# Performance work log

Measured on AMD Instinct MI355X. Metric: run time of the kernel, lower is better.

The kernel has to match this reference:

```python
import jax, jax.numpy as jnp
import numpy as np

H = 1024        # hidden_size
NH = 16         # num_heads
HD = H // NH    # head_dim
NS = 3          # num_strata


def setup_inputs() -> dict:
    key = jax.random.key(0)
    ks = jax.random.split(key, 12)
    s = 1.0 / np.sqrt(H)
    inp = {
        "hidden_states": jax.random.normal(ks[0], (2, 2048, H), dtype=jnp.float32),
        "Wq": jax.random.uniform(ks[1], (H, H), minval=-s, maxval=s, dtype=jnp.float32),
        "bq": jax.random.uniform(ks[2], (H,), minval=-s, maxval=s, dtype=jnp.float32),
        "Wk": jax.random.uniform(ks[3], (H, H), minval=-s, maxval=s, dtype=jnp.float32),
        "bk": jax.random.uniform(ks[4], (H,), minval=-s, maxval=s, dtype=jnp.float32),
        "Wv": jax.random.uniform(ks[5], (H, H), minval=-s, maxval=s, dtype=jnp.float32),
        "bv": jax.random.uniform(ks[6], (H,), minval=-s, maxval=s, dtype=jnp.float32),
        "Ws": jax.random.uniform(ks[7], (NS, H, H), minval=-s, maxval=s, dtype=jnp.float32),
        "bs": jax.random.uniform(ks[8], (NS, H), minval=-s, maxval=s, dtype=jnp.float32),
        "Wo": jax.random.uniform(ks[9], (H, H), minval=-s, maxval=s, dtype=jnp.float32),
        "bo": jax.random.uniform(ks[10], (H,), minval=-s, maxval=s, dtype=jnp.float32),
    }
    return inp


def reference(hidden_states, Wq, bq, Wk, bk, Wv, bv, Ws, bs, Wo, bo):
    B, S, _ = hidden_states.shape
    # torch nn.Linear: y = x @ W.T + b
    q = hidden_states @ Wq.T + bq
    k = hidden_states @ Wk.T + bk
    v = hidden_states @ Wv.T + bv
    # [B, NH, S, HD]
    q = q.reshape(B, S, NH, HD).transpose(0, 2, 1, 3)
    k = k.reshape(B, S, NH, HD).transpose(0, 2, 1, 3)
    v = v.reshape(B, S, NH, HD).transpose(0, 2, 1, 3)
    scores = jnp.einsum('bhqd,bhkd->bhqk', q, k) / jnp.sqrt(jnp.float32(HD))
    attn = jax.nn.softmax(scores, axis=-1)
    out = jnp.einsum('bhqk,bhkd->bhqd', attn, v)
    attn_output = out.transpose(0, 2, 1, 3).reshape(B, S, H)
    # stratum projections, averaged: [NS, B, S, H] -> mean over strata
    strata = jnp.einsum('bsh,ngh->nbsg', attn_output, Ws) + bs[:, None, None, :]
    enhanced = strata.mean(axis=0)
    output = enhanced @ Wo.T + bo
    return output
```

## Files before the change

### kernel.cpp

```cpp
#include <hip/hip_runtime.h>
#include <stdint.h>

typedef __attribute__((ext_vector_type(8))) short short8;
typedef __attribute__((ext_vector_type(4))) short short4v;
typedef __attribute__((ext_vector_type(4))) float f32x4;
typedef unsigned int u32;
typedef const __attribute__((address_space(1))) u32* gas_ptr;
typedef __attribute__((address_space(3))) u32* las_ptr;

__device__ inline short f2bf(float x) {
    u32 u = __float_as_uint(x);
    u = u + 0x7FFFu + ((u >> 16) & 1u);
    return (short)(u >> 16);
}
__device__ inline void gload16(const void* g, void* l) {
    __builtin_amdgcn_global_load_lds((gas_ptr)g, (las_ptr)l, 16, 0, 0);
}

__global__ __launch_bounds__(256) void prep(const float* __restrict__ X,
                                            const float* __restrict__ Wq,
                                            const float* __restrict__ Wk,
                                            const float* __restrict__ Wv,
                                            const float* __restrict__ Wo,
                                            const float* __restrict__ Ws,
                                            const float* __restrict__ bs,
                                            const float* __restrict__ bo,
                                            short* __restrict__ Xb,
                                            short* __restrict__ Wcat,
                                            short* __restrict__ Wob,
                                            short* __restrict__ WmT,
                                            float* __restrict__ bc) {
    __shared__ short T[64][65];
    const int tid = threadIdx.x;
    const int bid = blockIdx.x;
    if (bid < 8192) {
        const float* src;
        short* dst;
        int rel;
        if (bid < 4096)      { src = X;  dst = Xb;                rel = bid; }
        else if (bid < 5120) { src = Wq; dst = Wcat;              rel = bid - 4096; }
        else if (bid < 6144) { src = Wk; dst = Wcat + (1 << 20);  rel = bid - 5120; }
        else if (bid < 7168) { src = Wv; dst = Wcat + (2 << 20);  rel = bid - 6144; }
        else                 { src = Wo; dst = Wob;               rel = bid - 7168; }
        int i = (rel * 256 + tid) * 4;
        float4 v = *(const float4*)&src[i];
        short4v o;
        o[0] = f2bf(v.x); o[1] = f2bf(v.y); o[2] = f2bf(v.z); o[3] = f2bf(v.w);
        *(short4v*)&dst[i] = o;
    } else if (bid < 8448) {
        const int id = bid - 8192;
        const int gx = (id & 15) * 64, jy = (id >> 4) * 64;
        const int HH = 1 << 20;
        for (int e = tid; e < 4096; e += 256) {
            int j = e >> 6, g = e & 63;
            int idx = (jy + j) * 1024 + gx + g;
            float v = (Ws[idx] + Ws[idx + HH] + Ws[idx + 2 * HH]) * (1.0f / 3.0f);
            T[g][j] = f2bf(v);
        }
        __syncthreads();
        for (int e = tid; e < 4096; e += 256) {
            int g = e >> 6, j = e & 63;
            WmT[(long)(gx + g) * 1024 + jy + j] = T[g][j];
        }
    } else {
        const int lane = tid & 63;
        const int n = (bid - 8448) * 4 + (tid >> 6);
        float acc = 0.0f;
        for (int j0 = 0; j0 < 1024; j0 += 64) {
            int j = j0 + lane;
            float bm = (bs[j] + bs[j + 1024] + bs[j + 2048]) * (1.0f / 3.0f);
            acc += Wo[(long)n * 1024 + j] * bm;
        }
#pragma unroll
        for (int off = 1; off < 64; off <<= 1) acc += __shfl_xor(acc, off, 64);
        if (lane == 0) bc[n] = acc + bo[n];
    }
}

__global__ __launch_bounds__(256) void gemm_qkvwc(const short* __restrict__ Xb,
                                                  const short* __restrict__ Wcat,
                                                  const short* __restrict__ Wob,
                                                  const short* __restrict__ WmT,
                                                  const float* __restrict__ bq,
                                                  const float* __restrict__ bk,
                                                  const float* __restrict__ bv,
                                                  short* __restrict__ Qb,
                                                  short* __restrict__ Kb,
                                                  short* __restrict__ Vt,
                                                  short* __restrict__ Wc) {
    __shared__ short As[128 * 32];
    __shared__ short Bs[128 * 32];
    const int K = 1024;
    const int tid  = threadIdx.x;
    const int lane = tid & 63;
    const int wave = tid >> 6;
    const int quad = lane >> 4;
    const int l16  = lane & 15;
    const int bid = blockIdx.x;
    const short *A, *W;
    int m0, n0, sel;
    if (bid < 768) {
        m0 = (bid & 31) * 128;
        int t = bid >> 5;
        sel = t >> 3;
        n0 = (t & 7) * 128;
        A = Xb;
        W = Wcat + (long)sel * (1 << 20);
    } else {
        int w = bid - 768;
        sel = 3;
        m0 = (w >> 3) * 128;
        n0 = (w & 7) * 128;
        A = Wob;
        W = WmT;
    }
    const int wm = (wave >> 1) * 64;
    const int wn = (wave & 1) * 64;

    f32x4 acc[4][4] = {};
    const int r0 = tid >> 2, kk0 = (tid & 3) * 8;
    const int r1 = r0 + 64;

    for (int k0 = 0; k0 < K; k0 += 32) {
        gload16(&A[(long)(m0 + r0) * K + k0 + kk0], &As[wave * 512]);
        gload16(&A[(long)(m0 + r1) * K + k0 + kk0], &As[2048 + wave * 512]);
        gload16(&W[(long)(n0 + r0) * K + k0 + kk0], &Bs[wave * 512]);
        gload16(&W[(long)(n0 + r1) * K + k0 + kk0], &Bs[2048 + wave * 512]);
        __syncthreads();
        short8 af[4], bfr[4];
#pragma unroll
        for (int mi = 0; mi < 4; mi++)
            af[mi] = *(short8*)&As[(wm + mi * 16 + l16) * 32 + quad * 8];
#pragma unroll
        for (int ni = 0; ni < 4; ni++)
            bfr[ni] = *(short8*)&Bs[(wn + ni * 16 + l16) * 32 + quad * 8];
#pragma unroll
        for (int mi = 0; mi < 4; mi++)
#pragma unroll
            for (int ni = 0; ni < 4; ni++)
                acc[mi][ni] = __builtin_amdgcn_mfma_f32_16x16x32_bf16(af[mi], bfr[ni],
                                                                      acc[mi][ni], 0, 0, 0);
        __syncthreads();
    }

#pragma unroll
    for (int mi = 0; mi < 4; mi++) {
#pragma unroll
        for (int ni = 0; ni < 4; ni++) {
            const int n = n0 + wn + ni * 16 + l16;
            const int mbase = m0 + wm + mi * 16 + quad * 4;
            float bv2 = 0.0f;
            if (sel == 0) bv2 = bq[n];
            else if (sel == 1) bv2 = bk[n];
            else if (sel == 2) bv2 = bv[n];
            if (sel == 2) {
                short4v pk;
#pragma unroll
                for (int r = 0; r < 4; r++) pk[r] = f2bf(acc[mi][ni][r] + bv2);
                long addr = ((long)(mbase >> 11) << 21) + (long)n * 2048 + (mbase & 2047);
                *(short4v*)&Vt[addr] = pk;
            } else {
                short* C = (sel == 0) ? Qb : ((sel == 1) ? Kb : Wc);
#pragma unroll
                for (int r = 0; r < 4; r++)
                    C[(long)(mbase + r) * 1024 + n] = f2bf(acc[mi][ni][r] + bv2);
            }
        }
    }
}

__global__ __launch_bounds__(256) void attn_kernel(const short* __restrict__ Q,
                                                   const short* __restrict__ Kb,
                                                   const short* __restrict__ Vt,
                                                   short* __restrict__ O) {
    __shared__ short Ks[64 * 72];
    __shared__ short Vs[64 * 72];
    __shared__ short Ps[4 * 16 * 72];
    const int tid  = threadIdx.x;
    const int lane = tid & 63;
    const int wave = tid >> 6;
    const int quad = lane >> 4;
    const int l16  = lane & 15;
    const int q0 = blockIdx.x * 64;
    const int h  = blockIdx.y;
    const int b  = blockIdx.z;

    short8 qf[2];
    {
        long base = (long)(b * 2048 + q0 + wave * 16 + l16) * 1024 + h * 64 + quad * 8;
        qf[0] = *(const short8*)&Q[base];
        qf[1] = *(const short8*)&Q[base + 32];
    }

    const int sr0 = tid >> 3, sg0 = (tid & 7) * 8;
    const int sr1 = sr0 + 32;
    const short* Kp = Kb + (long)(b * 2048) * 1024 + h * 64;
    const short* Vp = Vt + ((long)b << 21) + (long)h * 64 * 2048;

    short8 pk0 = *(const short8*)&Kp[(long)sr0 * 1024 + sg0];
    short8 pk1 = *(const short8*)&Kp[(long)sr1 * 1024 + sg0];
    short8 pv0 = *(const short8*)&Vp[(long)sr0 * 2048 + sg0];
    short8 pv1 = *(const short8*)&Vp[(long)sr1 * 2048 + sg0];

    f32x4 o[4] = {};
    f32x4 ls = {};
    short8 ones;
#pragma unroll
    for (int j = 0; j < 8; j++) ones[j] = (short)0x3F80;

    for (int kt = 0; kt < 32; kt++) {
        *(short8*)&Ks[sr0 * 72 + sg0] = pk0;
        *(short8*)&Ks[sr1 * 72 + sg0] = pk1;
        *(short8*)&Vs[sr0 * 72 + sg0] = pv0;
        *(short8*)&Vs[sr1 * 72 + sg0] = pv1;
        __syncthreads();

        {
            const int kbn = ((kt + 1) & 31) * 64;
            pk0 = *(const short8*)&Kp[(long)(kbn + sr0) * 1024 + sg0];
            pk1 = *(const short8*)&Kp[(long)(kbn + sr1) * 1024 + sg0];
            pv0 = *(const short8*)&Vp[(long)sr0 * 2048 + kbn + sg0];
            pv1 = *(const short8*)&Vp[(long)sr1 * 2048 + kbn + sg0];
        }

        f32x4 s[4] = {};
#pragma unroll
        for (int ni = 0; ni < 4; ni++) {
            short8 bk0 = *(short8*)&Ks[(ni * 16 + l16) * 72 + quad * 8];
            short8 bk1 = *(short8*)&Ks[(ni * 16 + l16) * 72 + 32 + quad * 8];
            s[ni] = __builtin_amdgcn_mfma_f32_16x16x32_bf16(qf[0], bk0, s[ni], 0, 0, 0);
            s[ni] = __builtin_amdgcn_mfma_f32_16x16x32_bf16(qf[1], bk1, s[ni], 0, 0, 0);
        }

#pragma unroll
        for (int r = 0; r < 4; r++) {
            const int rowoff = wave * 1152 + (quad * 4 + r) * 72 + l16;
#pragma unroll
            for (int ni = 0; ni < 4; ni++) {
                float p = exp2f(s[ni][r] * 0.18033688011112042f);
                Ps[rowoff + ni * 16] = (short)((__float_as_uint(p) + 0x8000u) >> 16);
            }
        }

        short8 ap0 = *(short8*)&Ps[wave * 1152 + l16 * 72 + quad * 8];
        short8 ap1 = *(short8*)&Ps[wave * 1152 + l16 * 72 + 32 + quad * 8];
#pragma unroll
        for (int ni = 0; ni < 4; ni++) {
            short8 bv0 = *(short8*)&Vs[(ni * 16 + l16) * 72 + quad * 8];
            short8 bv1 = *(short8*)&Vs[(ni * 16 + l16) * 72 + 32 + quad * 8];
            o[ni] = __builtin_amdgcn_mfma_f32_16x16x32_bf16(ap0, bv0, o[ni], 0, 0, 0);
            o[ni] = __builtin_amdgcn_mfma_f32_16x16x32_bf16(ap1, bv1, o[ni], 0, 0, 0);
        }
        ls = __builtin_amdgcn_mfma_f32_16x16x32_bf16(ap0, ones, ls, 0, 0, 0);
        ls = __builtin_amdgcn_mfma_f32_16x16x32_bf16(ap1, ones, ls, 0, 0, 0);
        __syncthreads();
    }

#pragma unroll
    for (int r = 0; r < 4; r++) {
        const float inv = 1.0f / ls[r];
        const long row = (long)(b * 2048 + q0 + wave * 16 + quad * 4 + r) * 1024 + h * 64;
#pragma unroll
        for (int ni = 0; ni < 4; ni++)
            O[row + ni * 16 + l16] = f2bf(o[ni][r] * inv);
    }
}

__global__ __launch_bounds__(256) void gemm_final(const short* __restrict__ A,
                                                  const short* __restrict__ W,
                                                  const float* __restrict__ bias,
                                                  float* __restrict__ C) {
    __shared__ short As[64 * 32];
    __shared__ short Bs[128 * 32];
    const int K = 1024;
    const int tid  = threadIdx.x;
    const int lane = tid & 63;
    const int wave = tid >> 6;
    const int quad = lane >> 4;
    const int l16  = lane & 15;
    const int bid = blockIdx.x;
    const int m0 = (bid >> 3) * 64;
    const int n0 = (bid & 7) * 128;
    const int wm = (wave >> 1) * 32;
    const int wn = (wave & 1) * 64;

    f32x4 acc[2][4] = {};
    const int r0 = tid >> 2, kk0 = (tid & 3) * 8;

    for (int k0 = 0; k0 < K; k0 += 32) {
        gload16(&A[(long)(m0 + r0) * K + k0 + kk0], &As[wave * 512]);
        gload16(&W[(long)(n0 + r0) * K + k0 + kk0], &Bs[wave * 512]);
        gload16(&W[(long)(n0 + r0 + 64) * K + k0 + kk0], &Bs[2048 + wave * 512]);
        __syncthreads();
        short8 af[2], bfr[4];
#pragma unroll
        for (int mi = 0; mi < 2; mi++)
            af[mi] = *(short8*)&As[(wm + mi * 16 + l16) * 32 + quad * 8];
#pragma unroll
        for (int ni = 0; ni < 4; ni++)
            bfr[ni] = *(short8*)&Bs[(wn + ni * 16 + l16) * 32 + quad * 8];
#pragma unroll
        for (int mi = 0; mi < 2; mi++)
#pragma unroll
            for (int ni = 0; ni < 4; ni++)
                acc[mi][ni] = __builtin_amdgcn_mfma_f32_16x16x32_bf16(af[mi], bfr[ni],
                                                                      acc[mi][ni], 0, 0, 0);
        __syncthreads();
    }

#pragma unroll
    for (int mi = 0; mi < 2; mi++) {
#pragma unroll
        for (int ni = 0; ni < 4; ni++) {
            const int n = n0 + wn + ni * 16 + l16;
            const float bv = bias[n];
            const int mbase = m0 + wm + mi * 16 + quad * 4;
#pragma unroll
            for (int r = 0; r < 4; r++)
                C[(long)(mbase + r) * 1024 + n] = acc[mi][ni][r] + bv;
        }
    }
}

extern "C" void kernel_launch(void* const* d_in, const int* in_sizes, int n_in,
                              void* d_out, int out_size, void* d_ws, size_t ws_size,
                              hipStream_t stream) {
    const float* X  = (const float*)d_in[0];
    const float* Wq = (const float*)d_in[1];
    const float* bq = (const float*)d_in[2];
    const float* Wk = (const float*)d_in[3];
    const float* bk = (const float*)d_in[4];
    const float* Wv = (const float*)d_in[5];
    const float* bv = (const float*)d_in[6];
    const float* Ws = (const float*)d_in[7];
    const float* bs = (const float*)d_in[8];
    const float* Wo = (const float*)d_in[9];
    const float* bo = (const float*)d_in[10];

    char* ws = (char*)d_ws;
    const long MB = 1 << 20;
    short* Xb   = (short*)(ws + 0 * MB);
    short* Wcat = (short*)(ws + 8 * MB);
    short* WmT  = (short*)(ws + 14 * MB);
    short* Wob  = (short*)(ws + 16 * MB);
    short* Wc   = (short*)(ws + 18 * MB);
    float* bc   = (float*)(ws + 20 * MB);
    short* Qb   = (short*)(ws + 21 * MB);
    short* Kbf  = (short*)(ws + 29 * MB);
    short* Vtb  = (short*)(ws + 37 * MB);
    short* AO   = Xb;

    dim3 bb(256);

    prep<<<dim3(8704), bb, 0, stream>>>(X, Wq, Wk, Wv, Wo, Ws, bs, bo,
                                        Xb, Wcat, Wob, WmT, bc);
    gemm_qkvwc<<<dim3(832), bb, 0, stream>>>(Xb, Wcat, Wob, WmT, bq, bk, bv,
                                             Qb, Kbf, Vtb, Wc);
    attn_kernel<<<dim3(32, 16, 2), bb, 0, stream>>>(Qb, Kbf, Vtb, AO);
    gemm_final<<<dim3(512), bb, 0, stream>>>(AO, Wc, bc, (float*)d_out);
}
```

Baseline: 248.1 us.

## Fold softmax scale into Q, transpose score MFMA, widen GEMM K-tile

The QKV GEMM now stages 64-wide K slices per iteration, which halves the number of barrier pairs, and the softmax scale is applied once when Q is written. In attention, the score MFMA swaps its operands so each lane holds four consecutive keys of one query row. That lets P be packed with perm and written as 8-byte stores, and the row sum is accumulated in registers and reduced with shuffles instead of extra MFMAs against a ones vector. The risks are a larger shared-memory footprint in the GEMM and slightly different rounding from scaling Q before its bf16 conversion.

New measurement: 243.8 us. Within noise of the previous version (-1.7%).

```diff
diff --git a/kernel.cpp b/kernel.cpp
--- a/kernel.cpp
+++ b/kernel.cpp
@@ -4,9 +4,12 @@
 typedef __attribute__((ext_vector_type(8))) short short8;
 typedef __attribute__((ext_vector_type(4))) short short4v;
 typedef __attribute__((ext_vector_type(4))) float f32x4;
+typedef __attribute__((ext_vector_type(2))) unsigned int u32x2;
 typedef unsigned int u32;
 typedef const __attribute__((address_space(1))) u32* gas_ptr;
 typedef __attribute__((address_space(3))) u32* las_ptr;
+
+#define QSCALE 0.18033688011112042f
 
 __device__ inline short f2bf(float x) {
     u32 u = __float_as_uint(x);
@@ -88,8 +91,8 @@
                                                   short* __restrict__ Kb,
                                                   short* __restrict__ Vt,
                                                   short* __restrict__ Wc) {
-    __shared__ short As[128 * 32];
-    __shared__ short Bs[128 * 32];
+    __shared__ short As[128 * 64];
+    __shared__ short Bs[128 * 64];
     const int K = 1024;
     const int tid  = threadIdx.x;
     const int lane = tid & 63;
@@ -118,28 +121,33 @@
     const int wn = (wave & 1) * 64;
 
     f32x4 acc[4][4] = {};
-    const int r0 = tid >> 2, kk0 = (tid & 3) * 8;
-    const int r1 = r0 + 64;
-
-    for (int k0 = 0; k0 < K; k0 += 32) {
-        gload16(&A[(long)(m0 + r0) * K + k0 + kk0], &As[wave * 512]);
-        gload16(&A[(long)(m0 + r1) * K + k0 + kk0], &As[2048 + wave * 512]);
-        gload16(&W[(long)(n0 + r0) * K + k0 + kk0], &Bs[wave * 512]);
-        gload16(&W[(long)(n0 + r1) * K + k0 + kk0], &Bs[2048 + wave * 512]);
-        __syncthreads();
-        short8 af[4], bfr[4];
-#pragma unroll
-        for (int mi = 0; mi < 4; mi++)
-            af[mi] = *(short8*)&As[(wm + mi * 16 + l16) * 32 + quad * 8];
-#pragma unroll
-        for (int ni = 0; ni < 4; ni++)
-            bfr[ni] = *(short8*)&Bs[(wn + ni * 16 + l16) * 32 + quad * 8];
-#pragma unroll
-        for (int mi = 0; mi < 4; mi++)
-#pragma unroll
-            for (int ni = 0; ni < 4; ni++)
-                acc[mi][ni] = __builtin_amdgcn_mfma_f32_16x16x32_bf16(af[mi], bfr[ni],
+    const int srow = tid >> 3, scol = (tid & 7) * 8;
+
+    for (int k0 = 0; k0 < K; k0 += 64) {
+#pragma unroll
+        for (int i = 0; i < 4; i++) {
+            gload16(&A[(long)(m0 + i * 32 + srow) * K + k0 + scol], &As[i * 2048 + wave * 512]);
+            gload16(&W[(long)(n0 + i * 32 + srow) * K + k0 + scol], &Bs[i * 2048 + wave * 512]);
+        }
+        __syncthreads();
+        short8 bfr[4][2];
+#pragma unroll
+        for (int ni = 0; ni < 4; ni++) {
+            bfr[ni][0] = *(short8*)&Bs[(wn + ni * 16 + l16) * 64 + quad * 8];
+            bfr[ni][1] = *(short8*)&Bs[(wn + ni * 16 + l16) * 64 + 32 + quad * 8];
+        }
+#pragma unroll
+        for (int mi = 0; mi < 4; mi++) {
+            short8 af0 = *(short8*)&As[(wm + mi * 16 + l16) * 64 + quad * 8];
+            short8 af1 = *(short8*)&As[(wm + mi * 16 + l16) * 64 + 32 + quad * 8];
+#pragma unroll
+            for (int ni = 0; ni < 4; ni++) {
+                acc[mi][ni] = __builtin_amdgcn_mfma_f32_16x16x32_bf16(af0, bfr[ni][0],
                                                                       acc[mi][ni], 0, 0, 0);
+                acc[mi][ni] = __builtin_amdgcn_mfma_f32_16x16x32_bf16(af1, bfr[ni][1],
+                                                                      acc[mi][ni], 0, 0, 0);
+            }
+        }
         __syncthreads();
     }
 
@@ -159,8 +167,12 @@
                 for (int r = 0; r < 4; r++) pk[r] = f2bf(acc[mi][ni][r] + bv2);
                 long addr = ((long)(mbase >> 11) << 21) + (long)n * 2048 + (mbase & 2047);
                 *(short4v*)&Vt[addr] = pk;
+            } else if (sel == 0) {
+#pragma unroll
+                for (int r = 0; r < 4; r++)
+                    Qb[(long)(mbase + r) * 1024 + n] = f2bf((acc[mi][ni][r] + bv2) * QSCALE);
             } else {
-                short* C = (sel == 0) ? Qb : ((sel == 1) ? Kb : Wc);
+                short* C = (sel == 1) ? Kb : Wc;
 #pragma unroll
                 for (int r = 0; r < 4; r++)
                     C[(long)(mbase + r) * 1024 + n] = f2bf(acc[mi][ni][r] + bv2);
@@ -185,11 +197,11 @@
     const int h  = blockIdx.y;
     const int b  = blockIdx.z;
 
-    short8 qf[2];
+    short8 qf0, qf1;
     {
         long base = (long)(b * 2048 + q0 + wave * 16 + l16) * 1024 + h * 64 + quad * 8;
-        qf[0] = *(const short8*)&Q[base];
-        qf[1] = *(const short8*)&Q[base + 32];
+        qf0 = *(const short8*)&Q[base];
+        qf1 = *(const short8*)&Q[base + 32];
     }
 
     const int sr0 = tid >> 3, sg0 = (tid & 7) * 8;
@@ -203,10 +215,10 @@
     short8 pv1 = *(const short8*)&Vp[(long)sr1 * 2048 + sg0];
 
     f32x4 o[4] = {};
-    f32x4 ls = {};
-    short8 ones;
-#pragma unroll
-    for (int j = 0; j < 8; j++) ones[j] = (short)0x3F80;
+    float lsum = 0.0f;
+
+    u32* const pw = (u32*)&Ps[wave * 1152 + l16 * 72 + quad * 4];
+    const short* const pr = &Ps[wave * 1152 + l16 * 72 + quad * 8];
 
     for (int kt = 0; kt < 32; kt++) {
         *(short8*)&Ks[sr0 * 72 + sg0] = pk0;
@@ -223,27 +235,30 @@
             pv1 = *(const short8*)&Vp[(long)sr1 * 2048 + kbn + sg0];
         }
 
-        f32x4 s[4] = {};
-#pragma unroll
-        for (int ni = 0; ni < 4; ni++) {
-            short8 bk0 = *(short8*)&Ks[(ni * 16 + l16) * 72 + quad * 8];
-            short8 bk1 = *(short8*)&Ks[(ni * 16 + l16) * 72 + 32 + quad * 8];
-            s[ni] = __builtin_amdgcn_mfma_f32_16x16x32_bf16(qf[0], bk0, s[ni], 0, 0, 0);
-            s[ni] = __builtin_amdgcn_mfma_f32_16x16x32_bf16(qf[1], bk1, s[ni], 0, 0, 0);
-        }
-
-#pragma unroll
-        for (int r = 0; r < 4; r++) {
-            const int rowoff = wave * 1152 + (quad * 4 + r) * 72 + l16;
-#pragma unroll
-            for (int ni = 0; ni < 4; ni++) {
-                float p = exp2f(s[ni][r] * 0.18033688011112042f);
-                Ps[rowoff + ni * 16] = (short)((__float_as_uint(p) + 0x8000u) >> 16);
-            }
-        }
-
-        short8 ap0 = *(short8*)&Ps[wave * 1152 + l16 * 72 + quad * 8];
-        short8 ap1 = *(short8*)&Ps[wave * 1152 + l16 * 72 + 32 + quad * 8];
+#pragma unroll
+        for (int ni = 0; ni < 4; ni++) {
+            short8 ak0 = *(short8*)&Ks[(ni * 16 + l16) * 72 + quad * 8];
+            short8 ak1 = *(short8*)&Ks[(ni * 16 + l16) * 72 + 32 + quad * 8];
+            f32x4 s = {};
+            s = __builtin_amdgcn_mfma_f32_16x16x32_bf16(ak0, qf0, s, 0, 0, 0);
+            s = __builtin_amdgcn_mfma_f32_16x16x32_bf16(ak1, qf1, s, 0, 0, 0);
+            float p0 = __builtin_amdgcn_exp2f(s[0]);
+            float p1 = __builtin_amdgcn_exp2f(s[1]);
+            float p2 = __builtin_amdgcn_exp2f(s[2]);
+            float p3 = __builtin_amdgcn_exp2f(s[3]);
+            lsum += (p0 + p1) + (p2 + p3);
+            u32 a0 = __float_as_uint(p0) + 0x8000u;
+            u32 a1 = __float_as_uint(p1) + 0x8000u;
+            u32 a2 = __float_as_uint(p2) + 0x8000u;
+            u32 a3 = __float_as_uint(p3) + 0x8000u;
+            u32x2 w;
+            w[0] = __builtin_amdgcn_perm(a1, a0, 0x07060302u);
+            w[1] = __builtin_amdgcn_perm(a3, a2, 0x07060302u);
+            *(u32x2*)(pw + ni * 8) = w;
+        }
+
+        short8 ap0 = *(short8*)pr;
+        short8 ap1 = *(short8*)(pr + 32);
 #pragma unroll
         for (int ni = 0; ni < 4; ni++) {
             short8 bv0 = *(short8*)&Vs[(ni * 16 + l16) * 72 + quad * 8];
@@ -251,14 +266,15 @@
             o[ni] = __builtin_amdgcn_mfma_f32_16x16x32_bf16(ap0, bv0, o[ni], 0, 0, 0);
             o[ni] = __builtin_amdgcn_mfma_f32_16x16x32_bf16(ap1, bv1, o[ni], 0, 0, 0);
         }
-        ls = __builtin_amdgcn_mfma_f32_16x16x32_bf16(ap0, ones, ls, 0, 0, 0);
-        ls = __builtin_amdgcn_mfma_f32_16x16x32_bf16(ap1, ones, ls, 0, 0, 0);
-        __syncthreads();
-    }
-
+        __syncthreads();
+    }
+
+    lsum += __shfl_xor(lsum, 16, 64);
+    lsum += __shfl_xor(lsum, 32, 64);
 #pragma unroll
     for (int r = 0; r < 4; r++) {
-        const float inv = 1.0f / ls[r];
+        const float tot = __shfl(lsum, quad * 4 + r, 64);
+        const float inv = 1.0f / tot;
         const long row = (long)(b * 2048 + q0 + wave * 16 + quad * 4 + r) * 1024 + h * 64;
 #pragma unroll
         for (int ni = 0; ni < 4; ni++)
```
